# Kernel tuning notes

Hardware: AMD Instinct MI355X
Metric: run time of the kernel (lower is better)

The kernel has to match this reference:

```python
import jax, jax.numpy as jnp
import numpy as np


def setup_inputs() -> dict:
    key = jax.random.key(0)
    k1, k2, k3, k4, k5 = jax.random.split(key, 5)
    B, H, W, C = 4, 64, 64, 512
    ratio = 8
    d = C // ratio  # 64
    x = jax.random.normal(k1, (B, H, W, C), dtype=jnp.float32)
    # 1x1 conv weights (no bias) == channel-mixing matrices, he_normal-ish scale
    Wq = jax.random.normal(k2, (C, d), dtype=jnp.float32) * np.sqrt(2.0 / C)
    Wk = jax.random.normal(k3, (C, d), dtype=jnp.float32) * np.sqrt(2.0 / C)
    Wv = jax.random.normal(k4, (C, C), dtype=jnp.float32) * np.sqrt(2.0 / C)
    gamma = jax.random.normal(k5, (1,), dtype=jnp.float32)
    return {"x": x, "Wq": Wq, "Wk": Wk, "Wv": Wv, "gamma": gamma}


def reference(x, Wq, Wk, Wv, gamma):
    B, H, W, C = x.shape
    N = H * W
    # 1x1 convs (no bias) are per-pixel channel matmuls
    q = jnp.einsum('bhwc,cd->bhwd', x, Wq).reshape(B, N, -1)  # [B,N,d]
    k = jnp.einsum('bhwc,cd->bhwd', x, Wk).reshape(B, N, -1)  # [B,N,d]
    v = jnp.einsum('bhwc,cd->bhwd', x, Wv).reshape(B, N, C)   # [B,N,C]
    # energy[b,i,j] = key_i . query_j  (batch_dot(key, query^T))
    energy = jnp.einsum('bid,bjd->bij', k, q)                 # [B,N,N]
    attn = jax.nn.softmax(energy, axis=-1)
    out = jnp.einsum('bij,bjc->bic', attn, v)                 # [B,N,C]
    out = out.reshape(B, H, W, C)
    return gamma * out
```

## Files before the change

kernel.cpp:

```cpp
#include <hip/hip_runtime.h>
#include <hip/hip_bf16.h>

typedef unsigned short u16;
typedef unsigned int   u32;
typedef __attribute__((ext_vector_type(8))) short short8;
typedef __attribute__((ext_vector_type(4))) float f32x4;
typedef __attribute__((ext_vector_type(4))) u16   u16x4;

#define MFMA16(a,b,c) __builtin_amdgcn_mfma_f32_16x16x32_bf16((a),(b),(c),0,0,0)

#define BATCH 4
#define NPIX  4096
#define CCH   512
#define DDIM  64
#define MFIX  64.0f

static __device__ __forceinline__ u16 f2bf(float f){
  __hip_bfloat16 h = __float2bfloat16(f);
  return __builtin_bit_cast(u16, h);
}
static __device__ __forceinline__ float bf2f(u16 u){
  __hip_bfloat16 h = __builtin_bit_cast(__hip_bfloat16, u);
  return __bfloat162float(h);
}

__global__ __launch_bounds__(256) void k_wconv(const f32x4* __restrict__ wv,
                                               u16x4* __restrict__ wvb){
  const int i = blockIdx.x*256 + threadIdx.x;
  #pragma unroll
  for (int it=0; it<4; ++it){
    int idx = i + it*16384;
    f32x4 v = wv[idx];
    u16x4 o;
    o[0]=f2bf(v[0]); o[1]=f2bf(v[1]); o[2]=f2bf(v[2]); o[3]=f2bf(v[3]);
    wvb[idx] = o;
  }
}

__global__ __launch_bounds__(256) void k_qkproj(const float* __restrict__ x,
                                                const float* __restrict__ Wq,
                                                const float* __restrict__ Wk,
                                                u16* __restrict__ qhi, u16* __restrict__ qlo,
                                                u16* __restrict__ khi, u16* __restrict__ klo,
                                                u16* __restrict__ xhi){
  __shared__ float xs[32][512];
  const int pix0 = blockIdx.x * 32;
  {
    const f32x4* xg = (const f32x4*)(x + (size_t)pix0*CCH);
    f32x4* xsv = (f32x4*)(&xs[0][0]);
    #pragma unroll
    for (int it=0; it<16; ++it) xsv[threadIdx.x + it*256] = xg[threadIdx.x + it*256];
  }
  __syncthreads();
  #pragma unroll
  for (int e=0; e<16; ++e){
    int idx4 = e*256 + threadIdx.x;
    int f = idx4*4;
    int row = f >> 9, col = f & 511;
    f32x4 v = *(const f32x4*)(&xs[row][col]);
    u16x4 o;
    o[0]=f2bf(v[0]); o[1]=f2bf(v[1]); o[2]=f2bf(v[2]); o[3]=f2bf(v[3]);
    *(u16x4*)(&xhi[(size_t)(pix0+row)*CCH + col]) = o;
  }
  const int col = threadIdx.x & 127;
  const int grp = threadIdx.x >> 7;
  const float* W = (col < 64) ? Wq : Wk;
  const int wc = col & 63;
  float acc[16];
  #pragma unroll
  for (int p=0;p<16;++p) acc[p] = 0.f;
  #pragma unroll 2
  for (int c=0;c<512;c+=4){
    float w0 = W[(c+0)*64 + wc];
    float w1 = W[(c+1)*64 + wc];
    float w2 = W[(c+2)*64 + wc];
    float w3 = W[(c+3)*64 + wc];
    #pragma unroll
    for (int p=0;p<16;++p){
      f32x4 xv = *(const f32x4*)(&xs[grp*16+p][c]);
      acc[p] += xv[0]*w0 + xv[1]*w1 + xv[2]*w2 + xv[3]*w3;
    }
  }
  #pragma unroll
  for (int p=0;p<16;++p){
    int pix = pix0 + grp*16 + p;
    float v = acc[p];
    u16 hi = f2bf(v);
    u16 lo = f2bf(v - bf2f(hi));
    if (col < 64){ qhi[pix*64+wc] = hi; qlo[pix*64+wc] = lo; }
    else         { khi[pix*64+wc] = hi; klo[pix*64+wc] = lo; }
  }
}

__global__ __launch_bounds__(256) void k_vproj(const u16* __restrict__ xhi,
                                               const u16* __restrict__ wvb,
                                               u16* __restrict__ vT){
  __shared__ u16 As[64][72];
  __shared__ u16 Bs[64][266];
  const int pix0 = blockIdx.x * 64;
  const int c0   = blockIdx.y * 256;
  const int tid = threadIdx.x;
  const int w = tid >> 6, l = tid & 63;
  const int lg = l >> 4, ll = l & 15;
  f32x4 acc[4][4];
  #pragma unroll
  for (int mf=0;mf<4;++mf)
    #pragma unroll
    for (int nf=0;nf<4;++nf){ f32x4 z = {0.f,0.f,0.f,0.f}; acc[mf][nf] = z; }

  for (int ks=0; ks<8; ++ks){
    __syncthreads();
    #pragma unroll
    for (int it=0; it<2; ++it){
      int ch = tid + it*256; int r = ch>>3, c8 = ch&7;
      *(uint4*)(&As[r][c8*8]) = *(const uint4*)(&xhi[(size_t)(pix0+r)*CCH + ks*64 + c8*8]);
    }
    #pragma unroll
    for (int it=0; it<8; ++it){
      int ch = tid + it*256; int r = ch>>5, c32 = ch&31;
      uint4 d = *(const uint4*)(&wvb[(size_t)(ks*64+r)*CCH + c0 + c32*8]);
      u32* dst = (u32*)(&Bs[r][c32*8]);
      dst[0]=d.x; dst[1]=d.y; dst[2]=d.z; dst[3]=d.w;
    }
    __syncthreads();
    #pragma unroll
    for (int kc=0;kc<2;++kc){
      short8 a[4];
      #pragma unroll
      for (int mf=0;mf<4;++mf) a[mf] = *(const short8*)(&As[mf*16 + ll][kc*32 + lg*8]);
      #pragma unroll
      for (int nf=0;nf<4;++nf){
        short8 bb;
        int cc = w*64 + nf*16 + ll;
        #pragma unroll
        for (int e=0;e<8;++e) bb[e] = (short)Bs[kc*32 + lg*8 + e][cc];
        #pragma unroll
        for (int mf=0;mf<4;++mf) acc[mf][nf] = MFMA16(a[mf], bb, acc[mf][nf]);
      }
    }
  }
  #pragma unroll
  for (int mf=0;mf<4;++mf){
    #pragma unroll
    for (int nf=0;nf<4;++nf){
      int pix = pix0 + mf*16 + lg*4;
      int c   = c0 + w*64 + nf*16 + ll;
      u16x4 o;
      #pragma unroll
      for (int r=0;r<4;++r) o[r] = f2bf(acc[mf][nf][r]);
      size_t off = ((size_t)((pix>>12)*CCH + c))*NPIX + (pix & 4095);
      *(u16x4*)(vT + off) = o;
    }
  }
}

__global__ __launch_bounds__(512,4)
void k_attn(const u16* __restrict__ qhi, const u16* __restrict__ qlo,
            const u16* __restrict__ khi, const u16* __restrict__ klo,
            const u16* __restrict__ vT,  const float* __restrict__ gamma_p,
            float* __restrict__ out){
  __shared__ u16 Ps[2][64][72];
  __shared__ u16 Qs[2][64][72];
  const int bid = blockIdx.x;
  const int x  = bid & 7;
  const int b  = x >> 1, ch = x & 1;
  const int i0 = (bid >> 3) * 64;
  const int tid = threadIdx.x;
  const int w = tid >> 6, l = tid & 63;
  const int lg = l >> 4, ll = l & 15;
  const int iw = (w & 3) * 16;
  const int jw = (w >> 2) * 32;
  const int cw = ch*256 + w*32;

  const u16* qh_b  = qhi + (size_t)b*NPIX*DDIM;
  const u16* ql_b  = qlo + (size_t)b*NPIX*DDIM;
  const u16* vbase = vT  + (size_t)b*CCH*NPIX;

  short8 kfh[2], kfl[2];
  #pragma unroll
  for (int kc=0;kc<2;++kc){
    size_t a = ((size_t)(b*NPIX + i0 + iw + ll))*DDIM + kc*32 + lg*8;
    kfh[kc] = *(const short8*)(khi + a);
    kfl[kc] = *(const short8*)(klo + a);
  }
  short8 ones;
  #pragma unroll
  for (int e=0;e<8;++e) ones[e] = (short)0x3F80;

  f32x4 acc[4][2];
  #pragma unroll
  for (int mf=0;mf<4;++mf)
    #pragma unroll
    for (int nf=0;nf<2;++nf){ f32x4 z = {0.f,0.f,0.f,0.f}; acc[mf][nf] = z; }
  f32x4 accl[4];
  #pragma unroll
  for (int mf=0;mf<4;++mf){ f32x4 z = {0.f,0.f,0.f,0.f}; accl[mf] = z; }

  const int sc0   = tid*2;
  const int spart = sc0 >> 9;
  const int srow  = (sc0 >> 3) & 63;
  const int sq    = sc0 & 7;
  const u16* sgl  = spart ? ql_b : qh_b;
  uint4 qr0, qr1;

  auto stage_load = [&](int j0){
    const u16* p = sgl + (size_t)(j0 + srow)*DDIM + sq*8;
    qr0 = *(const uint4*)p;
    qr1 = *(const uint4*)(p + 8);
  };
  auto stage_write = [&](){
    u16* d = &Qs[spart][srow][sq*8];
    *(uint4*)d       = qr0;
    *(uint4*)(d + 8) = qr1;
  };

  auto s_step = [&](int buf){
    #pragma unroll
    for (int jf=0;jf<2;++jf){
      f32x4 s = {0.f,0.f,0.f,0.f};
      #pragma unroll
      for (int kc=0;kc<2;++kc){
        short8 qh = *(const short8*)(&Qs[0][jw + jf*16 + ll][kc*32 + lg*8]);
        short8 ql = *(const short8*)(&Qs[1][jw + jf*16 + ll][kc*32 + lg*8]);
        s = MFMA16(qh, kfh[kc], s);
        s = MFMA16(ql, kfh[kc], s);
        s = MFMA16(qh, kfl[kc], s);
      }
      u16x4 pk;
      #pragma unroll
      for (int r=0;r<4;++r) pk[r] = f2bf(__expf(s[r] - MFIX));
      *(u16x4*)(&Ps[buf][iw + ll][jw + jf*16 + lg*4]) = pk;
    }
  };

  stage_load(0);
  stage_write();
  stage_load(64);
  __syncthreads();
  s_step(0);

  for (int t=0; t<64; ++t){
    const int j0 = t*64;

    short8 vb[4];
    #pragma unroll
    for (int kc=0;kc<2;++kc)
      #pragma unroll
      for (int nf=0;nf<2;++nf)
        vb[kc*2+nf] = *(const short8*)(vbase + (size_t)(cw + nf*16 + ll)*NPIX + j0 + kc*32 + lg*8);

    __syncthreads();
    if (t < 63){
      stage_write();
      if (t < 62) stage_load(j0 + 128);
    }
    __syncthreads();
    if (t < 63) s_step((t+1)&1);

    #pragma unroll
    for (int kc=0;kc<2;++kc){
      short8 pa[4];
      #pragma unroll
      for (int mf=0;mf<4;++mf) pa[mf] = *(const short8*)(&Ps[t&1][mf*16 + ll][kc*32 + lg*8]);
      #pragma unroll
      for (int nf=0;nf<2;++nf)
        #pragma unroll
        for (int mf=0;mf<4;++mf) acc[mf][nf] = MFMA16(pa[mf], vb[kc*2+nf], acc[mf][nf]);
      #pragma unroll
      for (int mf=0;mf<4;++mf) accl[mf] = MFMA16(pa[mf], ones, accl[mf]);
    }
  }

  const float gm = gamma_p[0];
  #pragma unroll
  for (int mf=0;mf<4;++mf){
    f32x4 inv;
    #pragma unroll
    for (int r=0;r<4;++r) inv[r] = gm / accl[mf][r];
    #pragma unroll
    for (int nf=0;nf<2;++nf)
      #pragma unroll
      for (int r=0;r<4;++r){
        int row = i0 + mf*16 + lg*4 + r;
        int c   = cw + nf*16 + ll;
        out[((size_t)(b*NPIX + row))*CCH + c] = acc[mf][nf][r] * inv[r];
      }
  }
}

extern "C" void kernel_launch(void* const* d_in, const int* in_sizes, int n_in,
                              void* d_out, int out_size, void* d_ws, size_t ws_size,
                              hipStream_t stream) {
  (void)in_sizes; (void)n_in; (void)out_size; (void)ws_size;
  const float* x  = (const float*)d_in[0];
  const float* Wq = (const float*)d_in[1];
  const float* Wk = (const float*)d_in[2];
  const float* Wv = (const float*)d_in[3];
  const float* gm = (const float*)d_in[4];
  float* out = (float*)d_out;

  u16* qhi = (u16*)d_ws;
  u16* qlo = qhi + (size_t)BATCH*NPIX*DDIM;
  u16* khi = qlo + (size_t)BATCH*NPIX*DDIM;
  u16* klo = khi + (size_t)BATCH*NPIX*DDIM;
  u16* vT  = klo + (size_t)BATCH*NPIX*DDIM;

  u16* xhi = (u16*)d_out;
  u16* wvb = xhi + (size_t)BATCH*NPIX*CCH;

  k_qkproj<<<dim3(512), dim3(256), 0, stream>>>(x, Wq, Wk, qhi, qlo, khi, klo, xhi);
  k_wconv<<<dim3(64), dim3(256), 0, stream>>>((const f32x4*)Wv, (u16x4*)wvb);
  k_vproj<<<dim3(256,2), dim3(256), 0, stream>>>(xhi, wvb, vT);
  k_attn<<<dim3(512), dim3(512), 0, stream>>>(qhi, qlo, khi, klo, vT, gm, out);
}
```

Before: 235.1 us.

## Block V by key tile and compute softmax row sums in one wave

V is now stored in blocks of 64 keys, laid out [batch][key tile][channel][64]. Each attention step's V fragment is then one contiguous 64KB region instead of rows strided by NPIX, which should improve cache and TLB locality. The row-sum MFMA against a ones vector, previously repeated by all 8 waves, now runs only in wave 0. The sums are shared through LDS, which costs an extra barrier and some divergence between waves.

```diff
diff --git a/kernel.cpp b/kernel.cpp
--- a/kernel.cpp
+++ b/kernel.cpp
@@ -94,7 +94,7 @@
 
 __global__ __launch_bounds__(256) void k_vproj(const u16* __restrict__ xhi,
                                                const u16* __restrict__ wvb,
-                                               u16* __restrict__ vT){
+                                               u16* __restrict__ vJB){
   __shared__ u16 As[64][72];
   __shared__ u16 Bs[64][266];
   const int pix0 = blockIdx.x * 64;
@@ -145,11 +145,13 @@
     for (int nf=0;nf<4;++nf){
       int pix = pix0 + mf*16 + lg*4;
       int c   = c0 + w*64 + nf*16 + ll;
+      int bb  = pix >> 12;
+      int j   = pix & 4095;
       u16x4 o;
       #pragma unroll
       for (int r=0;r<4;++r) o[r] = f2bf(acc[mf][nf][r]);
-      size_t off = ((size_t)((pix>>12)*CCH + c))*NPIX + (pix & 4095);
-      *(u16x4*)(vT + off) = o;
+      size_t off = (((size_t)bb*64 + (j>>6))*CCH + c)*64 + (j&63);
+      *(u16x4*)(vJB + off) = o;
     }
   }
 }
@@ -157,10 +159,11 @@
 __global__ __launch_bounds__(512,4)
 void k_attn(const u16* __restrict__ qhi, const u16* __restrict__ qlo,
             const u16* __restrict__ khi, const u16* __restrict__ klo,
-            const u16* __restrict__ vT,  const float* __restrict__ gamma_p,
+            const u16* __restrict__ vJB, const float* __restrict__ gamma_p,
             float* __restrict__ out){
   __shared__ u16 Ps[2][64][72];
   __shared__ u16 Qs[2][64][72];
+  __shared__ float l_s[64];
   const int bid = blockIdx.x;
   const int x  = bid & 7;
   const int b  = x >> 1, ch = x & 1;
@@ -174,7 +177,7 @@
 
   const u16* qh_b  = qhi + (size_t)b*NPIX*DDIM;
   const u16* ql_b  = qlo + (size_t)b*NPIX*DDIM;
-  const u16* vbase = vT  + (size_t)b*CCH*NPIX;
+  const u16* vbase = vJB + (size_t)b*64*CCH*64;
 
   short8 kfh[2], kfl[2];
   #pragma unroll
@@ -240,19 +243,18 @@
   s_step(0);
 
   for (int t=0; t<64; ++t){
-    const int j0 = t*64;
-
+    const u16* vt = vbase + (size_t)t*CCH*64;
     short8 vb[4];
     #pragma unroll
     for (int kc=0;kc<2;++kc)
       #pragma unroll
       for (int nf=0;nf<2;++nf)
-        vb[kc*2+nf] = *(const short8*)(vbase + (size_t)(cw + nf*16 + ll)*NPIX + j0 + kc*32 + lg*8);
+        vb[kc*2+nf] = *(const short8*)(vt + (size_t)(cw + nf*16 + ll)*64 + kc*32 + lg*8);
 
     __syncthreads();
     if (t < 63){
       stage_write();
-      if (t < 62) stage_load(j0 + 128);
+      if (t < 62) stage_load(t*64 + 128);
     }
     __syncthreads();
     if (t < 63) s_step((t+1)&1);
@@ -266,17 +268,26 @@
       for (int nf=0;nf<2;++nf)
         #pragma unroll
         for (int mf=0;mf<4;++mf) acc[mf][nf] = MFMA16(pa[mf], vb[kc*2+nf], acc[mf][nf]);
-      #pragma unroll
-      for (int mf=0;mf<4;++mf) accl[mf] = MFMA16(pa[mf], ones, accl[mf]);
-    }
-  }
-
+      if (w == 0){
+        #pragma unroll
+        for (int mf=0;mf<4;++mf) accl[mf] = MFMA16(pa[mf], ones, accl[mf]);
+      }
+    }
+  }
+
+  if (w == 0 && ll == 0){
+    #pragma unroll
+    for (int mf=0;mf<4;++mf)
+      #pragma unroll
+      for (int r=0;r<4;++r) l_s[mf*16 + lg*4 + r] = accl[mf][r];
+  }
+  __syncthreads();
   const float gm = gamma_p[0];
   #pragma unroll
   for (int mf=0;mf<4;++mf){
     f32x4 inv;
     #pragma unroll
-    for (int r=0;r<4;++r) inv[r] = gm / accl[mf][r];
+    for (int r=0;r<4;++r) inv[r] = gm / l_s[mf*16 + lg*4 + r];
     #pragma unroll
     for (int nf=0;nf<2;++nf)
       #pragma unroll
@@ -303,13 +314,13 @@
   u16* qlo = qhi + (size_t)BATCH*NPIX*DDIM;
   u16* khi = qlo + (size_t)BATCH*NPIX*DDIM;
   u16* klo = khi + (size_t)BATCH*NPIX*DDIM;
-  u16* vT  = klo + (size_t)BATCH*NPIX*DDIM;
+  u16* vJB = klo + (size_t)BATCH*NPIX*DDIM;
 
   u16* xhi = (u16*)d_out;
   u16* wvb = xhi + (size_t)BATCH*NPIX*CCH;
 
   k_qkproj<<<dim3(512), dim3(256), 0, stream>>>(x, Wq, Wk, qhi, qlo, khi, klo, xhi);
   k_wconv<<<dim3(64), dim3(256), 0, stream>>>((const f32x4*)Wv, (u16x4*)wvb);
-  k_vproj<<<dim3(256,2), dim3(256), 0, stream>>>(xhi, wvb, vT);
-  k_attn<<<dim3(512), dim3(512), 0, stream>>>(qhi, qlo, khi, klo, vT, gm, out);
-}
+  k_vproj<<<dim3(256,2), dim3(256), 0, stream>>>(xhi, wvb, vJB);
+  k_attn<<<dim3(512), dim3(512), 0, stream>>>(qhi, qlo, khi, klo, vJB, gm, out);
+}
```

Result: faster. 224.5 us (-4.5%).
